# Kernel optimization log

Measured on AMD Instinct MI355X. Metric: run time of the kernel, lower is better.

The kernel has to match this reference:

```python
import jax, jax.numpy as jnp
import numpy as np

B, C, F, G, D, T = 4, 16, 35, 72, 24, 256

def setup_inputs() -> dict:
    key = jax.random.key(0)
    k1, k2, k3, k4, k5 = jax.random.split(key, 5)
    x_hat = jax.random.normal(k1, (B, C, F, D, D, D), dtype=jnp.float32)
    t = jax.random.normal(k2, (B, T), dtype=jnp.float32)
    # IFT matrix: group samples x irrep coefficients (normalized)
    A_ift = jax.random.normal(k3, (G, F), dtype=jnp.float32) / np.sqrt(F)
    # FT matrix: irrep coefficients x group samples (normalized)
    A_ft = jax.random.normal(k4, (F, G), dtype=jnp.float32) / np.sqrt(G)
    W_time = jax.random.normal(k5, (C, T), dtype=jnp.float32) * 0.02
    b_time = jnp.zeros((C,), dtype=jnp.float32)
    return {"x_hat": x_hat, "t": t, "A_ift": A_ift, "A_ft": A_ft,
            "W_time": W_time, "b_time": b_time}

def reference(x_hat, t, A_ift, A_ft, W_time, b_time):
    # Inverse group Fourier transform: coefficients -> samples on the group grid.
    # (B, C, F, D, D, D) -> (B, C, G, D, D, D)
    x = jnp.einsum('gf,bcfxyz->bcgxyz', A_ift, x_hat)
    # Time embedding -> per-channel bias (B, C)
    tb = t @ W_time.T + b_time
    # Bias add broadcast over (G, D, D, D) + elementwise SELU
    y = jax.nn.selu(x + tb[:, :, None, None, None, None])
    # Group Fourier transform back to coefficients: (B, C, F, D, D, D)
    return jnp.einsum('fg,bcgxyz->bcfxyz', A_ft, y)
```

## Files before the change

### kernel.cpp

```cpp
#include <hip/hip_runtime.h>
#include <hip/hip_bf16.h>

#define NB 4
#define NC 16
#define NF 35
#define NG 72
#define ND3 13824
#define NT 256

typedef __bf16 bf16x8 __attribute__((ext_vector_type(8)));
typedef float  f32x4  __attribute__((ext_vector_type(4)));
typedef unsigned int uint4v __attribute__((ext_vector_type(4)));
typedef unsigned short ushort_t;
typedef unsigned int   uint_t;

#define SELU_LAMBDA 1.0507009873554805f
#define SELU_LA     1.7580993408473766f


__device__ __forceinline__ ushort_t f2bf(float x) {
  uint_t u = __builtin_bit_cast(uint_t, x);
  u = (u + 0x7FFFu + ((u >> 16) & 1u)) >> 16;
  return (ushort_t)u;
}

__device__ __forceinline__ float selu_f(float v) {
  const float e   = __expf(v);
  const float neg = fmaf(SELU_LA, e, -SELU_LA);
  const float pos = SELU_LAMBDA * v;
  return (v > 0.0f) ? pos : neg;
}

__device__ __forceinline__ uint_t cvt_pk_bf16(float lo, float hi) {
  uint_t r;
  asm("v_cvt_pk_bf16_f32 %0, %1, %2" : "=v"(r) : "v"(lo), "v"(hi));
  return r;
}

__global__ __launch_bounds__(256) void fta_prep(
    const float* __restrict__ t, const float* __restrict__ A_ift,
    const float* __restrict__ A_ft, const float* __restrict__ W_time,
    const float* __restrict__ b_time, float* __restrict__ ws) {
  const int tid = threadIdx.x;
  if (tid < NB * NC) {
    const int b = tid / NC, c = tid % NC;
    float s = b_time[c];
    #pragma unroll 4
    for (int k = 0; k < NT; ++k) s = fmaf(t[b * NT + k], W_time[c * NT + k], s);
    ws[tid] = s;
  }
  ushort_t* A1 = (ushort_t*)(ws + 64);
  ushort_t* A2 = A1 + 80 * 64;
  for (int i = tid; i < 80 * 64; i += 256) {
    const int g = i >> 6, f = i & 63;
    A1[i] = (g < NG && f < NF) ? f2bf(A_ift[g * NF + f]) : (ushort_t)0;
  }
  for (int i = tid; i < 48 * 96; i += 256) {
    const int fp = i / 96, g = i % 96;
    A2[i] = (fp < NF && g < NG) ? f2bf(A_ft[fp * NG + g]) : (ushort_t)0;
  }
}

__global__ __launch_bounds__(256, 4) void fta_mfma(
    const float* __restrict__ x_hat, const float* __restrict__ ws,
    float* __restrict__ out) {
  __shared__ __align__(16) ushort_t Ys[4][16][104];

  const int tid  = threadIdx.x;
  const int w    = tid >> 6;
  const int lane = tid & 63;
  const int v16  = lane & 15;
  const int q    = lane >> 4;
  const int bc   = blockIdx.y;

  const float tb = ws[bc];
  const ushort_t* __restrict__ A1p = (const ushort_t*)(ws + 64);
  const ushort_t* __restrict__ A2p = A1p + 80 * 64;

  bf16x8 a1[5][2];
  #pragma unroll
  for (int mt = 0; mt < 5; ++mt)
    #pragma unroll
    for (int ks = 0; ks < 2; ++ks)
      a1[mt][ks] = *(const bf16x8*)(A1p + (16 * mt + v16) * 64 + 32 * ks + 8 * q);

  {
    uint_t* yz = (uint_t*)&Ys[w][0][0];
    #pragma unroll 1
    for (int i = lane; i < 832; i += 64) yz[i] = 0;
  }
  ushort_t (* __restrict__ Yw)[104] = Ys[w];

  const float* __restrict__ xbase =
      x_hat + (size_t)bc * (NF * ND3) + blockIdx.x * 256 + w * 64 + v16;
  float* __restrict__ obase =
      out + (size_t)bc * (NF * ND3) + blockIdx.x * 256 + w * 64 + v16;

  float xrA[8], xtA[3], xrB[8], xtB[3];

  auto LOADX = [&](float (&xr)[8], float (&xt)[3], int it) {
    const float* __restrict__ xp = xbase + it * 16;
    #pragma unroll
    for (int i = 0; i < 8; ++i) xr[i] = xp[(size_t)(8 * q + i) * ND3];
    xt[0] = xt[1] = xt[2] = 0.0f;
    if (q == 0) {
      #pragma unroll
      for (int i = 0; i < 3; ++i) xt[i] = xp[(size_t)(32 + i) * ND3];
    }
  };

  auto COMPUTE = [&](const float (&xr)[8], const float (&xt)[3], int it) {
    uint4v u0;
    u0.x = cvt_pk_bf16(xr[0], xr[1]);
    u0.y = cvt_pk_bf16(xr[2], xr[3]);
    u0.z = cvt_pk_bf16(xr[4], xr[5]);
    u0.w = cvt_pk_bf16(xr[6], xr[7]);
    uint4v u1;
    u1.x = cvt_pk_bf16(xt[0], xt[1]);
    u1.y = cvt_pk_bf16(xt[2], 0.0f);
    u1.z = 0; u1.w = 0;
    const bf16x8 bx0 = __builtin_bit_cast(bf16x8, u0);
    const bf16x8 bx1 = __builtin_bit_cast(bf16x8, u1);

    f32x4 acc[5];
    #pragma unroll
    for (int mt = 0; mt < 5; ++mt) acc[mt] = (f32x4){tb, tb, tb, tb};
    #pragma unroll
    for (int mt = 0; mt < 5; ++mt) {
      acc[mt] = __builtin_amdgcn_mfma_f32_16x16x32_bf16(a1[mt][0], bx0, acc[mt], 0, 0, 0);
      acc[mt] = __builtin_amdgcn_mfma_f32_16x16x32_bf16(a1[mt][1], bx1, acc[mt], 0, 0, 0);
    }

    #pragma unroll
    for (int mt = 0; mt < 5; ++mt) {
      const bool wr = (mt < 4) || (q < 2);
      #pragma unroll
      for (int jp = 0; jp < 2; ++jp) {
        const float y0 = selu_f(acc[mt][2 * jp + 0]);
        const float y1 = selu_f(acc[mt][2 * jp + 1]);
        const uint_t pk = cvt_pk_bf16(y0, y1);
        if (wr) *(uint_t*)&Yw[v16][16 * mt + 4 * q + 2 * jp] = pk;
      }
    }

    f32x4 o[3];
    #pragma unroll
    for (int m2 = 0; m2 < 3; ++m2) o[m2] = (f32x4){0.f, 0.f, 0.f, 0.f};
    #pragma unroll
    for (int ks2 = 0; ks2 < 3; ++ks2) {
      const bf16x8 by = *(const bf16x8*)&Yw[v16][32 * ks2 + 8 * q];
      #pragma unroll
      for (int m2 = 0; m2 < 3; ++m2) {
        const bf16x8 a2 = *(const bf16x8*)(A2p + (16 * m2 + v16) * 96 + 32 * ks2 + 8 * q);
        o[m2] = __builtin_amdgcn_mfma_f32_16x16x32_bf16(a2, by, o[m2], 0, 0, 0);
      }
    }

    float* __restrict__ op = obase + it * 16;
    #pragma unroll
    for (int m2 = 0; m2 < 3; ++m2)
      #pragma unroll
      for (int j = 0; j < 4; ++j) {
        const int fp = 16 * m2 + 4 * q + j;
        if (fp < NF) op[(size_t)fp * ND3] = o[m2][j];
      }
  };

  LOADX(xrA, xtA, 0);
  LOADX(xrB, xtB, 1);
  COMPUTE(xrA, xtA, 0);
  LOADX(xrA, xtA, 2);
  COMPUTE(xrB, xtB, 1);
  LOADX(xrB, xtB, 3);
  COMPUTE(xrA, xtA, 2);
  COMPUTE(xrB, xtB, 3);
}

extern "C" void kernel_launch(void* const* d_in, const int* in_sizes, int n_in,
                              void* d_out, int out_size, void* d_ws, size_t ws_size,
                              hipStream_t stream) {
  const float* x_hat  = (const float*)d_in[0];
  const float* t      = (const float*)d_in[1];
  const float* A_ift  = (const float*)d_in[2];
  const float* A_ft   = (const float*)d_in[3];
  const float* W_time = (const float*)d_in[4];
  const float* b_time = (const float*)d_in[5];
  float* out = (float*)d_out;
  float* ws  = (float*)d_ws;

  fta_prep<<<1, 256, 0, stream>>>(t, A_ift, A_ft, W_time, b_time, ws);

  dim3 grid(ND3 / 256, NB * NC);
  fta_mfma<<<grid, 256, 0, stream>>>(x_hat, ws, out);
}
```

Measured before the change: 74.60 us.

## Stage transform matrices in LDS, fold SELU lambda into A_ft, raise occupancy

The padded bf16 A_ift and A_ft matrices are copied from the workspace into shared memory once per block. A_ift fragments are then read from LDS instead of being held in registers, and A_ft fragments are read from LDS instead of global memory. The SELU scale lambda is folded into A_ft during prep, and the Y buffer is shrunk so the third k-step re-reads valid rows instead of relying on zeroed padding. Together with launch bounds raised to 5 waves per SIMD, this aims to cut register pressure and global traffic, at the cost of more LDS per block, an extra __syncthreads, and extra LDS reads per tile.

```diff
diff --git a/kernel.cpp b/kernel.cpp
--- a/kernel.cpp
+++ b/kernel.cpp
@@ -15,20 +15,15 @@
 typedef unsigned int   uint_t;
 
 #define SELU_LAMBDA 1.0507009873554805f
-#define SELU_LA     1.7580993408473766f
+#define SELU_ALPHA  1.6732632423543772f
 
+#define A1_LD 72
+#define A2_LD 104
 
 __device__ __forceinline__ ushort_t f2bf(float x) {
   uint_t u = __builtin_bit_cast(uint_t, x);
   u = (u + 0x7FFFu + ((u >> 16) & 1u)) >> 16;
   return (ushort_t)u;
-}
-
-__device__ __forceinline__ float selu_f(float v) {
-  const float e   = __expf(v);
-  const float neg = fmaf(SELU_LA, e, -SELU_LA);
-  const float pos = SELU_LAMBDA * v;
-  return (v > 0.0f) ? pos : neg;
 }
 
 __device__ __forceinline__ uint_t cvt_pk_bf16(float lo, float hi) {
@@ -49,22 +44,24 @@
     for (int k = 0; k < NT; ++k) s = fmaf(t[b * NT + k], W_time[c * NT + k], s);
     ws[tid] = s;
   }
-  ushort_t* A1 = (ushort_t*)(ws + 64);
-  ushort_t* A2 = A1 + 80 * 64;
-  for (int i = tid; i < 80 * 64; i += 256) {
-    const int g = i >> 6, f = i & 63;
-    A1[i] = (g < NG && f < NF) ? f2bf(A_ift[g * NF + f]) : (ushort_t)0;
+  ushort_t* A1g = (ushort_t*)(ws + 64);
+  ushort_t* A2g = A1g + 80 * A1_LD;
+  for (int i = tid; i < 80 * A1_LD; i += 256) {
+    const int g = i / A1_LD, f = i % A1_LD;
+    A1g[i] = (g < NG && f < NF) ? f2bf(A_ift[g * NF + f]) : (ushort_t)0;
   }
-  for (int i = tid; i < 48 * 96; i += 256) {
-    const int fp = i / 96, g = i % 96;
-    A2[i] = (fp < NF && g < NG) ? f2bf(A_ft[fp * NG + g]) : (ushort_t)0;
+  for (int i = tid; i < 48 * A2_LD; i += 256) {
+    const int fp = i / A2_LD, g = i % A2_LD;
+    A2g[i] = (fp < NF && g < NG) ? f2bf(SELU_LAMBDA * A_ft[fp * NG + g]) : (ushort_t)0;
   }
 }
 
-__global__ __launch_bounds__(256, 4) void fta_mfma(
+__global__ __launch_bounds__(256, 5) void fta_mfma(
     const float* __restrict__ x_hat, const float* __restrict__ ws,
     float* __restrict__ out) {
-  __shared__ __align__(16) ushort_t Ys[4][16][104];
+  __shared__ __align__(16) ushort_t Ys[4][16][88];
+  __shared__ __align__(16) ushort_t A1L[80 * A1_LD];
+  __shared__ __align__(16) ushort_t A2L[48 * A2_LD];
 
   const int tid  = threadIdx.x;
   const int w    = tid >> 6;
@@ -74,22 +71,22 @@
   const int bc   = blockIdx.y;
 
   const float tb = ws[bc];
-  const ushort_t* __restrict__ A1p = (const ushort_t*)(ws + 64);
-  const ushort_t* __restrict__ A2p = A1p + 80 * 64;
-
-  bf16x8 a1[5][2];
-  #pragma unroll
-  for (int mt = 0; mt < 5; ++mt)
-    #pragma unroll
-    for (int ks = 0; ks < 2; ++ks)
-      a1[mt][ks] = *(const bf16x8*)(A1p + (16 * mt + v16) * 64 + 32 * ks + 8 * q);
+  const ushort_t* __restrict__ A1g = (const ushort_t*)(ws + 64);
+  const ushort_t* __restrict__ A2g = A1g + 80 * A1_LD;
 
   {
-    uint_t* yz = (uint_t*)&Ys[w][0][0];
+    const uint4v* s1 = (const uint4v*)A1g;
+    uint4v* d1 = (uint4v*)A1L;
     #pragma unroll 1
-    for (int i = lane; i < 832; i += 64) yz[i] = 0;
+    for (int i = tid; i < 80 * A1_LD / 8; i += 256) d1[i] = s1[i];
+    const uint4v* s2 = (const uint4v*)A2g;
+    uint4v* d2 = (uint4v*)A2L;
+    #pragma unroll 1
+    for (int i = tid; i < 48 * A2_LD / 8; i += 256) d2[i] = s2[i];
   }
-  ushort_t (* __restrict__ Yw)[104] = Ys[w];
+  __syncthreads();
+
+  ushort_t (* __restrict__ Yw)[88] = Ys[w];
 
   const float* __restrict__ xbase =
       x_hat + (size_t)bc * (NF * ND3) + blockIdx.x * 256 + w * 64 + v16;
@@ -127,19 +124,21 @@
     for (int mt = 0; mt < 5; ++mt) acc[mt] = (f32x4){tb, tb, tb, tb};
     #pragma unroll
     for (int mt = 0; mt < 5; ++mt) {
-      acc[mt] = __builtin_amdgcn_mfma_f32_16x16x32_bf16(a1[mt][0], bx0, acc[mt], 0, 0, 0);
-      acc[mt] = __builtin_amdgcn_mfma_f32_16x16x32_bf16(a1[mt][1], bx1, acc[mt], 0, 0, 0);
+      const bf16x8 a1k0 = *(const bf16x8*)&A1L[(16 * mt + v16) * A1_LD + 8 * q];
+      const bf16x8 a1k1 = *(const bf16x8*)&A1L[(16 * mt + v16) * A1_LD + 32 + 8 * q];
+      acc[mt] = __builtin_amdgcn_mfma_f32_16x16x32_bf16(a1k0, bx0, acc[mt], 0, 0, 0);
+      acc[mt] = __builtin_amdgcn_mfma_f32_16x16x32_bf16(a1k1, bx1, acc[mt], 0, 0, 0);
     }
 
     #pragma unroll
     for (int mt = 0; mt < 5; ++mt) {
-      const bool wr = (mt < 4) || (q < 2);
       #pragma unroll
       for (int jp = 0; jp < 2; ++jp) {
-        const float y0 = selu_f(acc[mt][2 * jp + 0]);
-        const float y1 = selu_f(acc[mt][2 * jp + 1]);
-        const uint_t pk = cvt_pk_bf16(y0, y1);
-        if (wr) *(uint_t*)&Yw[v16][16 * mt + 4 * q + 2 * jp] = pk;
+        const float v0 = acc[mt][2 * jp + 0];
+        const float v1 = acc[mt][2 * jp + 1];
+        const float y0 = (v0 > 0.0f) ? v0 : fmaf(SELU_ALPHA, __expf(v0), -SELU_ALPHA);
+        const float y1 = (v1 > 0.0f) ? v1 : fmaf(SELU_ALPHA, __expf(v1), -SELU_ALPHA);
+        *(uint_t*)&Yw[v16][16 * mt + 4 * q + 2 * jp] = cvt_pk_bf16(y0, y1);
       }
     }
 
@@ -148,10 +147,11 @@
     for (int m2 = 0; m2 < 3; ++m2) o[m2] = (f32x4){0.f, 0.f, 0.f, 0.f};
     #pragma unroll
     for (int ks2 = 0; ks2 < 3; ++ks2) {
-      const bf16x8 by = *(const bf16x8*)&Yw[v16][32 * ks2 + 8 * q];
+      const int rowoff = (ks2 < 2) ? (32 * ks2 + 8 * q) : (64 + 8 * (q & 1));
+      const bf16x8 by = *(const bf16x8*)&Yw[v16][rowoff];
       #pragma unroll
       for (int m2 = 0; m2 < 3; ++m2) {
-        const bf16x8 a2 = *(const bf16x8*)(A2p + (16 * m2 + v16) * 96 + 32 * ks2 + 8 * q);
+        const bf16x8 a2 = *(const bf16x8*)&A2L[(16 * m2 + v16) * A2_LD + 32 * ks2 + 8 * q];
         o[m2] = __builtin_amdgcn_mfma_f32_16x16x32_bf16(a2, by, o[m2], 0, 0, 0);
       }
     }
```

New measurement: 181.9 us. 2.44x slower.
